# Kernel optimization log

Measured on AMD Instinct MI355X. Metric: run time of the kernel, lower is better.

Reference implementation:

```python
import jax, jax.numpy as jnp
import numpy as np

T, K, N = 4096, 4096, 11008  # tokens, in_features, out_features


def _unpack_int4(packed):
    """packed: int8 [..., K//2] -> signed 4-bit values int8 [..., K].
    Low nibble first, high nibble second; arithmetic shifts sign-extend."""
    lo = jnp.right_shift(jnp.left_shift(packed, 4).astype(jnp.int8), 4)
    hi = jnp.right_shift(packed, 4).astype(jnp.int8)
    out = jnp.stack([lo, hi], axis=-1)  # [..., K//2, 2]
    return out.reshape(*packed.shape[:-1], packed.shape[-1] * 2)


def _pack_int4(vals):
    """vals: int8 in [-8,7], [..., K] -> packed int8 [..., K//2]."""
    v = vals.reshape(*vals.shape[:-1], vals.shape[-1] // 2, 2)
    lo = v[..., 0] & 0xF
    hi = v[..., 1] & 0xF
    return (lo | jnp.left_shift(hi, 4)).astype(jnp.int8)


def setup_inputs() -> dict:
    key = jax.random.key(0)
    k1, k2, k3, k4 = jax.random.split(key, 4)
    # symmetric 4-bit quantized values in [-7, 7], packed two per byte
    x_int = jax.random.randint(k1, (T, K), -7, 8).astype(jnp.int8)
    w_int = jax.random.randint(k2, (N, K), -7, 8).astype(jnp.int8)
    pq_x = _pack_int4(x_int)
    weight = _pack_int4(w_int)
    # per-token / per-output-channel dequant scales (max_abs/7 style magnitudes)
    scales_x = (jax.random.uniform(k3, (T,), jnp.float32) * 0.01 + 1e-4)
    weight_scales = (jax.random.uniform(k4, (N,), jnp.float32) * 0.01 + 1e-4)
    return {"pq_x": pq_x, "scales_x": scales_x, "weight": weight,
            "weight_scales": weight_scales}


def reference(pq_x, scales_x, weight, weight_scales):
    # Unpack int4 operands. Products |a*w| <= 49 and K=4096 => |acc| <= 2e5,
    # exactly representable in fp32, so the fp32 matmul equals int32 GEMM.
    a = _unpack_int4(pq_x).astype(jnp.float32)      # [T, K]
    w = _unpack_int4(weight).astype(jnp.float32)    # [N, K]
    acc = jnp.einsum('tk,nk->tn', a, w)             # integer GEMM in fp32
    # fused per-token x per-output-channel dequant
    out = acc * scales_x[:, None] * weight_scales[None, :]
    out = out.astype(jnp.float16)
    return out[None]  # unsqueeze(0) as in the torch module
```

## Files before the change

### kernel.cpp

```cpp
#include <hip/hip_runtime.h>
#include <hip/hip_fp16.h>
#include <stdint.h>


#define T_DIM 4096
#define K_DIM 4096
#define N_DIM 11008
#define KP    2048
#define BM 128
#define BN 256
#define STAGES 64
#define A_PANELS (T_DIM / BM)
#define B_PANELS (N_DIM / BN)
#define CHUNK_A 8192
#define CHUNK_B 16384
#define WS_A ((size_t)A_PANELS * STAGES * CHUNK_A)
#define WS_B ((size_t)B_PANELS * STAGES * CHUNK_B)
#define NA_BYTES ((size_t)T_DIM * KP)
#define NW_BYTES ((size_t)N_DIM * KP)

typedef __attribute__((ext_vector_type(4)))  int int32x4;
typedef __attribute__((ext_vector_type(16))) int int32x16;
typedef __attribute__((ext_vector_type(4)))  float floatx4;
typedef __attribute__((ext_vector_type(8)))  _Float16 f16x8;
typedef __attribute__((ext_vector_type(2)))  _Float16 f16x2;

__device__ __forceinline__ uint32_t pack4(int4 v) {
  return (uint32_t)(v.x & 0xFF) | ((uint32_t)(v.y & 0xFF) << 8) |
         ((uint32_t)(v.z & 0xFF) << 16) | ((uint32_t)(v.w & 0xFF) << 24);
}
__device__ __forceinline__ uint32_t nib_lo_s8(uint32_t p) {
  uint32_t t = (p & 0x0F0F0F0Fu) ^ 0x88888888u;
  return (t - 0x08080808u) ^ 0x80808080u;
}
__device__ __forceinline__ uint32_t nib_hi_s8(uint32_t p) {
  uint32_t t = ((p >> 4) & 0x0F0F0F0Fu) ^ 0x88888888u;
  return (t - 0x08080808u) ^ 0x80808080u;
}

#define ROWS_PB 32
#define SGRP    16

__global__ __launch_bounds__(256) void unpack_tiles3(
    const int* __restrict__ xa, const int* __restrict__ xw,
    uint8_t* __restrict__ wsa, uint8_t* __restrict__ wsb)
{
  __shared__ __align__(16) uint32_t lds[8192];
  const int sg  = blockIdx.x;
  const int yb  = blockIdx.y;
  const int tid = threadIdx.x;

  const int* srcBase; uint8_t* dstBase; int cellStride, chunkStride;
  if (yb < T_DIM / ROWS_PB) {
    srcBase = xa + (size_t)yb * ROWS_PB * KP + sg * SGRP * 32;
    dstBase = wsa + ((size_t)(yb >> 2) * STAGES + sg * SGRP) * CHUNK_A
                  + (size_t)(yb & 3) * (ROWS_PB * 16);
    cellStride = 2048; chunkStride = CHUNK_A;
  } else {
    const int zb = yb - T_DIM / ROWS_PB;
    srcBase = xw + (size_t)zb * ROWS_PB * KP + sg * SGRP * 32;
    dstBase = wsb + ((size_t)(zb >> 3) * STAGES + sg * SGRP) * CHUNK_B
                  + (size_t)(zb & 7) * (ROWS_PB * 16);
    cellStride = 4096; chunkStride = CHUNK_B;
  }

  const int lq    = tid & 127;
  const int rhalf = tid >> 7;
  const int sl    = lq >> 3;
  const int tg    = lq & 7;
  const int cellL = (tg & 1) * 2;
  const int dsl   = tg >> 1;
#pragma unroll
  for (int it = 0; it < 16; ++it) {
    const int row = it * 2 + rhalf;
    const int4 v = *(const int4*)(srcBase + (size_t)row * KP + lq * 4);
    const uint32_t p = pack4(v);
    const int sp = sl ^ (row & 7);
    uint32_t* b = &lds[(((cellL * 32 + row) << 4) + sp) * 4 + dsl];
    b[0]    = nib_lo_s8(p);
    b[2048] = nib_hi_s8(p);
  }
  __syncthreads();

  const int row2 = tid & 31;
#pragma unroll
  for (int it = 0; it < 8; ++it) {
    const int pr = it * 8 + (tid >> 5);
    const int s2 = pr >> 2, cl = pr & 3;
    const int sp = s2 ^ (row2 & 7);
    const uint4 v = *(const uint4*)&lds[(((cl * 32 + row2) << 4) + sp) * 4];
    *(uint4*)(dstBase + (size_t)s2 * chunkStride + cl * cellStride + row2 * 16) = v;
  }
}

__device__ __forceinline__ void dma16(const uint8_t* g, uint8_t* l) {
  __builtin_amdgcn_global_load_lds(
      (const __attribute__((address_space(1))) uint32_t*)g,
      (__attribute__((address_space(3))) uint32_t*)l, 16, 0, 0);
}

__global__ __launch_bounds__(512, 4) void gemm_i8_tb2(
    const uint8_t* __restrict__ wsa, const uint8_t* __restrict__ wsb,
    const float* __restrict__ sx, const float* __restrict__ sw,
    float* __restrict__ out)
{
  __shared__ __align__(16) uint8_t sAmem[3 * CHUNK_A];
  __shared__ __align__(16) uint8_t sBmem[3 * CHUNK_B];

  const int tid  = threadIdx.x;
  const int lane = tid & 63;
  const int wv   = tid >> 6;
  const int wm   = wv >> 2, wn = wv & 3;
  const int h    = lane >> 5;
  const int ml   = lane & 31;
  const int pp   = blockIdx.x;
  const int qq   = blockIdx.y;

  const uint8_t* chunkA = wsa + (size_t)pp * STAGES * CHUNK_A;
  const uint8_t* chunkB = wsb + (size_t)qq * STAGES * CHUNK_B;
  const int laneOff = lane * 16;
  const int aOffW   = wv * 1024;
  const int bOffW   = wv * 2048;

  const int rowA = (wm * 64 + ml) * 16;
  const int rowB = (wn * 64 + ml) * 16;

  int32x16 acc[2][2];
#pragma unroll
  for (int mi = 0; mi < 2; ++mi)
#pragma unroll
    for (int ni = 0; ni < 2; ++ni)
#pragma unroll
      for (int i = 0; i < 16; ++i) acc[mi][ni][i] = 0;

  auto dma_stage = [&](int s, int buf) {
    const uint8_t* ca = chunkA + (size_t)s * CHUNK_A;
    const uint8_t* cb = chunkB + (size_t)s * CHUNK_B;
    uint8_t* la = sAmem + buf * CHUNK_A;
    uint8_t* lb = sBmem + buf * CHUNK_B;
    dma16(ca + aOffW + laneOff,        la + aOffW);
    dma16(cb + bOffW + laneOff,        lb + bOffW);
    dma16(cb + bOffW + 1024 + laneOff, lb + bOffW + 1024);
  };

  dma_stage(0, 0);
  dma_stage(1, 1);

  int rb = 0;
  int wb = 2;
#pragma unroll 1
  for (int s = 0; s < STAGES; ++s) {
    if (s < STAGES - 1) asm volatile("s_waitcnt vmcnt(3)" ::: "memory");
    else                asm volatile("s_waitcnt vmcnt(0)" ::: "memory");
    __builtin_amdgcn_s_barrier();
    if (s + 2 < STAGES) dma_stage(s + 2, wb);

    const uint8_t* baseA = sAmem + rb * CHUNK_A;
    const uint8_t* baseB = sBmem + rb * CHUNK_B;
#pragma unroll
    for (int s2 = 0; s2 < 2; ++s2) {
      const int c = 2 * s2 + h;
      const uint8_t* pa = baseA + c * 2048 + rowA;
      const uint8_t* pb = baseB + c * 4096 + rowB;
      int32x4 aF[2], bF[2];
#pragma unroll
      for (int mi = 0; mi < 2; ++mi) aF[mi] = *(const int32x4*)(pa + mi * 512);
#pragma unroll
      for (int ni = 0; ni < 2; ++ni) bF[ni] = *(const int32x4*)(pb + ni * 512);
      __builtin_amdgcn_s_setprio(1);
#pragma unroll
      for (int mi = 0; mi < 2; ++mi)
#pragma unroll
        for (int ni = 0; ni < 2; ++ni)
          acc[mi][ni] = __builtin_amdgcn_mfma_i32_32x32x32_i8(
              aF[mi], bF[ni], acc[mi][ni], 0, 0, 0);
      __builtin_amdgcn_s_setprio(0);
    }
    rb = (rb == 2) ? 0 : rb + 1;
    wb = (wb == 2) ? 0 : wb + 1;
  }

#pragma unroll
  for (int mi = 0; mi < 2; ++mi) {
    const int rbase = pp * BM + wm * 64 + mi * 32 + 4 * h;
    float sxv[16];
#pragma unroll
    for (int r = 0; r < 16; ++r) sxv[r] = sx[rbase + (r & 3) + 8 * (r >> 2)];
#pragma unroll
    for (int ni = 0; ni < 2; ++ni) {
      const int gcol = qq * BN + wn * 64 + ni * 32 + ml;
      const float swv = sw[gcol];
#pragma unroll
      for (int r = 0; r < 16; ++r) {
        const int grow = rbase + (r & 3) + 8 * (r >> 2);
        const float v = (float)acc[mi][ni][r] * sxv[r] * swv;
        out[(size_t)grow * N_DIM + gcol] = __half2float(__float2half(v));
      }
    }
  }
}

__global__ __launch_bounds__(256) void repack_int32_to_bytes(
    const int* __restrict__ xa, const int* __restrict__ xw,
    uint32_t* __restrict__ da, uint32_t* __restrict__ dw)
{
  const size_t i = (size_t)blockIdx.x * blockDim.x + threadIdx.x;
  const size_t na4 = NA_BYTES / 4;
  const int4* src; uint32_t* dst; size_t off;
  if (i < na4) { src = (const int4*)xa; dst = da; off = i; }
  else         { src = (const int4*)xw; dst = dw; off = i - na4; }
  const int4 v = src[off];
  dst[off] = pack4(v);
}

__device__ __forceinline__ uint32_t cvt2(uint32_t m) {
  union U { uint32_t u; f16x2 h; } a, b, c;
  a.u = m ^ 0x64086408u; b.u = 0xE408E408u; c.h = a.h + b.h;
  return c.u;
}
__device__ __forceinline__ void unpack_cell(uint32_t* cell, uint32_t p) {
  cell[0] = cvt2( p        & 0x000F000Fu);
  cell[1] = cvt2((p >> 4)  & 0x000F000Fu);
  cell[2] = cvt2((p >> 8)  & 0x000F000Fu);
  cell[3] = cvt2((p >> 12) & 0x000F000Fu);
}

template <bool PACKED>
__global__ __launch_bounds__(256) void linear4bit_f16(
    const uint8_t* __restrict__ pqx, const float* __restrict__ sx,
    const uint8_t* __restrict__ wq,  const float* __restrict__ sw,
    const int* __restrict__ pqx32,   const int* __restrict__ wq32,
    float* __restrict__ out)
{
  __shared__ uint32_t sAf[8][128][4];
  __shared__ uint32_t sBf[8][128][4];
  const int tid = threadIdx.x, lane = tid & 63, wv = tid >> 6;
  const int wm = wv >> 1, wn = wv & 1, qd = lane >> 4, m16 = lane & 15;
  const int bm0 = blockIdx.x * 128, bn0 = blockIdx.y * 128;
  const int srow = tid >> 1, sh = tid & 1;
  const uint8_t* aPtr = pqx + (size_t)(bm0 + srow) * KP + sh * 16;
  const uint8_t* bPtr = wq  + (size_t)(bn0 + srow) * KP + sh * 16;
  const int* aPtr32 = pqx32 + (size_t)(bm0 + srow) * KP + sh * 16;
  const int* bPtr32 = wq32  + (size_t)(bn0 + srow) * KP + sh * 16;
  floatx4 acc[4][4];
#pragma unroll
  for (int mi = 0; mi < 4; ++mi)
#pragma unroll
    for (int ni = 0; ni < 4; ++ni)
#pragma unroll
      for (int r = 0; r < 4; ++r) acc[mi][ni][r] = 0.0f;
  uint4 ar, br;
  auto load_stage = [&](int s) {
    if (PACKED) {
      ar = *(const uint4*)(aPtr + (size_t)s * 32);
      br = *(const uint4*)(bPtr + (size_t)s * 32);
    } else {
      const int4* a4 = (const int4*)(aPtr32 + (size_t)s * 32);
      const int4* b4 = (const int4*)(bPtr32 + (size_t)s * 32);
      ar.x = pack4(a4[0]); ar.y = pack4(a4[1]); ar.z = pack4(a4[2]); ar.w = pack4(a4[3]);
      br.x = pack4(b4[0]); br.y = pack4(b4[1]); br.z = pack4(b4[2]); br.w = pack4(b4[3]);
    }
  };
  auto stage_to_lds = [&]() {
    uint32_t pa[4] = {ar.x, ar.y, ar.z, ar.w};
    uint32_t pb[4] = {br.x, br.y, br.z, br.w};
#pragma unroll
    for (int i = 0; i < 4; ++i) {
      unpack_cell(&sAf[4 * sh + i][srow][0], pa[i]);
      unpack_cell(&sBf[4 * sh + i][srow][0], pb[i]);
    }
  };
  load_stage(0); stage_to_lds();
#pragma unroll 1
  for (int s = 0; s < STAGES; ++s) {
    __syncthreads();
    if (s + 1 < STAGES) load_stage(s + 1);
#pragma unroll
    for (int s2 = 0; s2 < 2; ++s2) {
      f16x8 aF[4], bF[4];
#pragma unroll
      for (int mi = 0; mi < 4; ++mi)
        aF[mi] = *(const f16x8*)&sAf[4 * s2 + qd][wm * 64 + mi * 16 + m16][0];
#pragma unroll
      for (int ni = 0; ni < 4; ++ni)
        bF[ni] = *(const f16x8*)&sBf[4 * s2 + qd][wn * 64 + ni * 16 + m16][0];
#pragma unroll
      for (int mi = 0; mi < 4; ++mi)
#pragma unroll
        for (int ni = 0; ni < 4; ++ni)
          acc[mi][ni] = __builtin_amdgcn_mfma_f32_16x16x32_f16(aF[mi], bF[ni], acc[mi][ni], 0, 0, 0);
    }
    __syncthreads();
    if (s + 1 < STAGES) stage_to_lds();
  }
#pragma unroll
  for (int mi = 0; mi < 4; ++mi) {
    const int grow0 = bm0 + wm * 64 + mi * 16 + qd * 4;
    const float s0 = sx[grow0], s1 = sx[grow0 + 1], s2v = sx[grow0 + 2], s3 = sx[grow0 + 3];
#pragma unroll
    for (int ni = 0; ni < 4; ++ni) {
      const int gcol = bn0 + wn * 64 + ni * 16 + m16;
      const float swv = sw[gcol];
      const floatx4 a = acc[mi][ni];
      out[(size_t)(grow0 + 0) * N_DIM + gcol] = __half2float(__float2half(a[0] * s0 * swv));
      out[(size_t)(grow0 + 1) * N_DIM + gcol] = __half2float(__float2half(a[1] * s1 * swv));
      out[(size_t)(grow0 + 2) * N_DIM + gcol] = __half2float(__float2half(a[2] * s2v * swv));
      out[(size_t)(grow0 + 3) * N_DIM + gcol] = __half2float(__float2half(a[3] * s3 * swv));
    }
  }
}

extern "C" void kernel_launch(void* const* d_in, const int* in_sizes, int n_in,
                              void* d_out, int out_size, void* d_ws, size_t ws_size,
                              hipStream_t stream) {
  const int*   pqx32 = (const int*)d_in[0];
  const float* sxp   = (const float*)d_in[1];
  const int*   wq32  = (const int*)d_in[2];
  const float* swp   = (const float*)d_in[3];
  float* outp = (float*)d_out;

  if (ws_size >= WS_A + WS_B) {
    uint8_t* wsa = (uint8_t*)d_ws;
    uint8_t* wsb = wsa + WS_A;
    unpack_tiles3<<<dim3(STAGES / SGRP, T_DIM / ROWS_PB + N_DIM / ROWS_PB), 256, 0, stream>>>(
        pqx32, wq32, wsa, wsb);
    gemm_i8_tb2<<<dim3(A_PANELS, B_PANELS), 512, 0, stream>>>(wsa, wsb, sxp, swp, outp);
  } else if (ws_size >= NA_BYTES + NW_BYTES) {
    uint8_t* da = (uint8_t*)d_ws;
    uint8_t* dw = da + NA_BYTES;
    const size_t total4 = (NA_BYTES + NW_BYTES) / 4;
    repack_int32_to_bytes<<<(uint32_t)(total4 / 256), 256, 0, stream>>>(
        pqx32, wq32, (uint32_t*)da, (uint32_t*)dw);
    linear4bit_f16<true><<<dim3(T_DIM / 128, N_DIM / 128), 256, 0, stream>>>(
        da, sxp, dw, swp, nullptr, nullptr, outp);
  } else {
    linear4bit_f16<false><<<dim3(T_DIM / 128, N_DIM / 128), 256, 0, stream>>>(
        nullptr, sxp, nullptr, swp, pqx32, wq32, outp);
  }
}
```

Before: 466.8 us.

## Use 4-wave blocks with 2x4 warp tiles and phased DMA/MFMA interleaving

Cuts the GEMM block from 8 to 4 waves, so each wave now computes a 64x128 tile (2x4 MFMA accumulators) rather than 64x64. This gives more register reuse of A fragments. The stage loop is split into four phases, and each phase interleaves a few global-to-LDS DMA issues with one group of MFMAs, separated by extra barriers. The aim is to spread memory traffic across compute, but the extra barriers and the halved thread count per block could lower latency hiding and occupancy.

```diff
diff --git a/kernel.cpp b/kernel.cpp
--- a/kernel.cpp
+++ b/kernel.cpp
@@ -99,7 +99,7 @@
       (__attribute__((address_space(3))) uint32_t*)l, 16, 0, 0);
 }
 
-__global__ __launch_bounds__(512, 4) void gemm_i8_tb2(
+__global__ __launch_bounds__(256, 2) void gemm_i8_ph(
     const uint8_t* __restrict__ wsa, const uint8_t* __restrict__ wsb,
     const float* __restrict__ sx, const float* __restrict__ sw,
     float* __restrict__ out)
@@ -110,7 +110,7 @@
   const int tid  = threadIdx.x;
   const int lane = tid & 63;
   const int wv   = tid >> 6;
-  const int wm   = wv >> 2, wn = wv & 3;
+  const int wm   = wv >> 1, wn = wv & 1;
   const int h    = lane >> 5;
   const int ml   = lane & 31;
   const int pp   = blockIdx.x;
@@ -118,64 +118,102 @@
 
   const uint8_t* chunkA = wsa + (size_t)pp * STAGES * CHUNK_A;
   const uint8_t* chunkB = wsb + (size_t)qq * STAGES * CHUNK_B;
-  const int laneOff = lane * 16;
-  const int aOffW   = wv * 1024;
-  const int bOffW   = wv * 2048;
+  const int segOff = wv * 1024 + lane * 16;
+  const int ldsOff = wv * 1024;
 
   const int rowA = (wm * 64 + ml) * 16;
-  const int rowB = (wn * 64 + ml) * 16;
-
-  int32x16 acc[2][2];
+  const int rowB = (wn * 128 + ml) * 16;
+
+  int32x16 acc[2][4];
 #pragma unroll
   for (int mi = 0; mi < 2; ++mi)
 #pragma unroll
-    for (int ni = 0; ni < 2; ++ni)
+    for (int ni = 0; ni < 4; ++ni)
 #pragma unroll
       for (int i = 0; i < 16; ++i) acc[mi][ni][i] = 0;
 
-  auto dma_stage = [&](int s, int buf) {
-    const uint8_t* ca = chunkA + (size_t)s * CHUNK_A;
-    const uint8_t* cb = chunkB + (size_t)s * CHUNK_B;
-    uint8_t* la = sAmem + buf * CHUNK_A;
-    uint8_t* lb = sBmem + buf * CHUNK_B;
-    dma16(ca + aOffW + laneOff,        la + aOffW);
-    dma16(cb + bOffW + laneOff,        lb + bOffW);
-    dma16(cb + bOffW + 1024 + laneOff, lb + bOffW + 1024);
+  auto dmaA = [&](int s, int buf, int i) {
+    dma16(chunkA + (size_t)s * CHUNK_A + segOff + i * 4096,
+          sAmem + buf * CHUNK_A + ldsOff + i * 4096);
   };
-
-  dma_stage(0, 0);
-  dma_stage(1, 1);
+  auto dmaB = [&](int s, int buf, int i) {
+    dma16(chunkB + (size_t)s * CHUNK_B + segOff + i * 4096,
+          sBmem + buf * CHUNK_B + ldsOff + i * 4096);
+  };
+
+  dmaA(0, 0, 0); dmaA(0, 0, 1);
+  dmaB(0, 0, 0); dmaB(0, 0, 1); dmaB(0, 0, 2); dmaB(0, 0, 3);
+  dmaA(1, 1, 0); dmaA(1, 1, 1);
+  dmaB(1, 1, 0); dmaB(1, 1, 1); dmaB(1, 1, 2); dmaB(1, 1, 3);
 
   int rb = 0;
   int wb = 2;
 #pragma unroll 1
   for (int s = 0; s < STAGES; ++s) {
-    if (s < STAGES - 1) asm volatile("s_waitcnt vmcnt(3)" ::: "memory");
+    if (s < STAGES - 1) asm volatile("s_waitcnt vmcnt(6)" ::: "memory");
     else                asm volatile("s_waitcnt vmcnt(0)" ::: "memory");
     __builtin_amdgcn_s_barrier();
-    if (s + 2 < STAGES) dma_stage(s + 2, wb);
+    const bool pf = (s + 2 < STAGES);
 
     const uint8_t* baseA = sAmem + rb * CHUNK_A;
     const uint8_t* baseB = sBmem + rb * CHUNK_B;
-#pragma unroll
-    for (int s2 = 0; s2 < 2; ++s2) {
-      const int c = 2 * s2 + h;
-      const uint8_t* pa = baseA + c * 2048 + rowA;
-      const uint8_t* pb = baseB + c * 4096 + rowB;
-      int32x4 aF[2], bF[2];
-#pragma unroll
-      for (int mi = 0; mi < 2; ++mi) aF[mi] = *(const int32x4*)(pa + mi * 512);
-#pragma unroll
-      for (int ni = 0; ni < 2; ++ni) bF[ni] = *(const int32x4*)(pb + ni * 512);
-      __builtin_amdgcn_s_setprio(1);
-#pragma unroll
-      for (int mi = 0; mi < 2; ++mi)
-#pragma unroll
-        for (int ni = 0; ni < 2; ++ni)
-          acc[mi][ni] = __builtin_amdgcn_mfma_i32_32x32x32_i8(
-              aF[mi], bF[ni], acc[mi][ni], 0, 0, 0);
-      __builtin_amdgcn_s_setprio(0);
-    }
+    const uint8_t* paL = baseA + h * 2048 + rowA;
+    const uint8_t* pbL = baseB + h * 4096 + rowB;
+    const uint8_t* paH = baseA + (2 + h) * 2048 + rowA;
+    const uint8_t* pbH = baseB + (2 + h) * 4096 + rowB;
+
+    int32x4 a0, a1, b0, b1;
+
+    a0 = *(const int32x4*)(paL);
+    a1 = *(const int32x4*)(paL + 512);
+    b0 = *(const int32x4*)(pbL);
+    b1 = *(const int32x4*)(pbL + 512);
+    if (pf) { dmaA(s + 2, wb, 0); dmaA(s + 2, wb, 1); }
+    __builtin_amdgcn_s_barrier();
+    __builtin_amdgcn_s_setprio(1);
+    acc[0][0] = __builtin_amdgcn_mfma_i32_32x32x32_i8(a0, b0, acc[0][0], 0, 0, 0);
+    acc[1][0] = __builtin_amdgcn_mfma_i32_32x32x32_i8(a1, b0, acc[1][0], 0, 0, 0);
+    acc[0][1] = __builtin_amdgcn_mfma_i32_32x32x32_i8(a0, b1, acc[0][1], 0, 0, 0);
+    acc[1][1] = __builtin_amdgcn_mfma_i32_32x32x32_i8(a1, b1, acc[1][1], 0, 0, 0);
+    __builtin_amdgcn_s_setprio(0);
+    __builtin_amdgcn_s_barrier();
+
+    b0 = *(const int32x4*)(pbL + 1024);
+    b1 = *(const int32x4*)(pbL + 1536);
+    if (pf) { dmaB(s + 2, wb, 0); dmaB(s + 2, wb, 1); }
+    __builtin_amdgcn_s_barrier();
+    __builtin_amdgcn_s_setprio(1);
+    acc[0][2] = __builtin_amdgcn_mfma_i32_32x32x32_i8(a0, b0, acc[0][2], 0, 0, 0);
+    acc[1][2] = __builtin_amdgcn_mfma_i32_32x32x32_i8(a1, b0, acc[1][2], 0, 0, 0);
+    acc[0][3] = __builtin_amdgcn_mfma_i32_32x32x32_i8(a0, b1, acc[0][3], 0, 0, 0);
+    acc[1][3] = __builtin_amdgcn_mfma_i32_32x32x32_i8(a1, b1, acc[1][3], 0, 0, 0);
+    __builtin_amdgcn_s_setprio(0);
+    __builtin_amdgcn_s_barrier();
+
+    a0 = *(const int32x4*)(paH);
+    a1 = *(const int32x4*)(paH + 512);
+    b0 = *(const int32x4*)(pbH);
+    b1 = *(const int32x4*)(pbH + 512);
+    if (pf) { dmaB(s + 2, wb, 2); dmaB(s + 2, wb, 3); }
+    __builtin_amdgcn_s_barrier();
+    __builtin_amdgcn_s_setprio(1);
+    acc[0][0] = __builtin_amdgcn_mfma_i32_32x32x32_i8(a0, b0, acc[0][0], 0, 0, 0);
+    acc[1][0] = __builtin_amdgcn_mfma_i32_32x32x32_i8(a1, b0, acc[1][0], 0, 0, 0);
+    acc[0][1] = __builtin_amdgcn_mfma_i32_32x32x32_i8(a0, b1, acc[0][1], 0, 0, 0);
+    acc[1][1] = __builtin_amdgcn_mfma_i32_32x32x32_i8(a1, b1, acc[1][1], 0, 0, 0);
+    __builtin_amdgcn_s_setprio(0);
+    __builtin_amdgcn_s_barrier();
+
+    b0 = *(const int32x4*)(pbH + 1024);
+    b1 = *(const int32x4*)(pbH + 1536);
+    __builtin_amdgcn_s_barrier();
+    __builtin_amdgcn_s_setprio(1);
+    acc[0][2] = __builtin_amdgcn_mfma_i32_32x32x32_i8(a0, b0, acc[0][2], 0, 0, 0);
+    acc[1][2] = __builtin_amdgcn_mfma_i32_32x32x32_i8(a1, b0, acc[1][2], 0, 0, 0);
+    acc[0][3] = __builtin_amdgcn_mfma_i32_32x32x32_i8(a0, b1, acc[0][3], 0, 0, 0);
+    acc[1][3] = __builtin_amdgcn_mfma_i32_32x32x32_i8(a1, b1, acc[1][3], 0, 0, 0);
+    __builtin_amdgcn_s_setprio(0);
+
     rb = (rb == 2) ? 0 : rb + 1;
     wb = (wb == 2) ? 0 : wb + 1;
   }
@@ -187,8 +225,8 @@
 #pragma unroll
     for (int r = 0; r < 16; ++r) sxv[r] = sx[rbase + (r & 3) + 8 * (r >> 2)];
 #pragma unroll
-    for (int ni = 0; ni < 2; ++ni) {
-      const int gcol = qq * BN + wn * 64 + ni * 32 + ml;
+    for (int ni = 0; ni < 4; ++ni) {
+      const int gcol = qq * BN + wn * 128 + ni * 32 + ml;
       const float swv = sw[gcol];
 #pragma unroll
       for (int r = 0; r < 16; ++r) {
@@ -324,7 +362,7 @@
     uint8_t* wsb = wsa + WS_A;
     unpack_tiles3<<<dim3(STAGES / SGRP, T_DIM / ROWS_PB + N_DIM / ROWS_PB), 256, 0, stream>>>(
         pqx32, wq32, wsa, wsb);
-    gemm_i8_tb2<<<dim3(A_PANELS, B_PANELS), 512, 0, stream>>>(wsa, wsb, sxp, swp, outp);
+    gemm_i8_ph<<<dim3(A_PANELS, B_PANELS), 256, 0, stream>>>(wsa, wsb, sxp, swp, outp);
   } else if (ws_size >= NA_BYTES + NW_BYTES) {
     uint8_t* da = (uint8_t*)d_ws;
     uint8_t* dw = da + NA_BYTES;
```

After: 469.2 us. No clear change (+0.5%).

## Use 256x256 tiles with 4 waves, 4-deep LDS pipeline and XCD-aware block swizzle

Applied to the files above, without the earlier changes.

Replaces the 128x256 tile GEMM (8 waves, 3-stage buffers) with a 256x256 tile handled by 4 waves, each computing a 128x128 sub-tile of 4x4 MFMA accumulators. Stages are quadruple-buffered, with DMA issued three stages ahead and LDS fragment loads double-buffered in registers so reads overlap the MFMA blocks. Block indices are swizzled across 8 groups so that neighbouring tiles share the same chiplet's L2. The unpack kernel is changed to write A in the same 16 KB chunk layout as B. The larger tile raises reuse per byte loaded, at the cost of very high register pressure and one block per CU.

```diff
diff --git a/kernel.cpp b/kernel.cpp
--- a/kernel.cpp
+++ b/kernel.cpp
@@ -7,15 +7,16 @@
 #define K_DIM 4096
 #define N_DIM 11008
 #define KP    2048
-#define BM 128
-#define BN 256
 #define STAGES 64
-#define A_PANELS (T_DIM / BM)
-#define B_PANELS (N_DIM / BN)
-#define CHUNK_A 8192
-#define CHUNK_B 16384
-#define WS_A ((size_t)A_PANELS * STAGES * CHUNK_A)
-#define WS_B ((size_t)B_PANELS * STAGES * CHUNK_B)
+#define BM2 256
+#define BN2 256
+#define CHUNK2 16384
+#define A_PANELS2 (T_DIM / BM2)
+#define B_PANELS2 (N_DIM / BN2)
+#define NWG2 (A_PANELS2 * B_PANELS2)
+#define CPX2 (NWG2 / 8)
+#define WS_A ((size_t)A_PANELS2 * STAGES * CHUNK2)
+#define WS_B ((size_t)B_PANELS2 * STAGES * CHUNK2)
 #define NA_BYTES ((size_t)T_DIM * KP)
 #define NW_BYTES ((size_t)N_DIM * KP)
 
@@ -41,7 +42,7 @@
 #define ROWS_PB 32
 #define SGRP    16
 
-__global__ __launch_bounds__(256) void unpack_tiles3(
+__global__ __launch_bounds__(256) void unpack_tiles4(
     const int* __restrict__ xa, const int* __restrict__ xw,
     uint8_t* __restrict__ wsa, uint8_t* __restrict__ wsb)
 {
@@ -50,18 +51,16 @@
   const int yb  = blockIdx.y;
   const int tid = threadIdx.x;
 
-  const int* srcBase; uint8_t* dstBase; int cellStride, chunkStride;
+  const int* srcBase; uint8_t* dstBase;
   if (yb < T_DIM / ROWS_PB) {
     srcBase = xa + (size_t)yb * ROWS_PB * KP + sg * SGRP * 32;
-    dstBase = wsa + ((size_t)(yb >> 2) * STAGES + sg * SGRP) * CHUNK_A
-                  + (size_t)(yb & 3) * (ROWS_PB * 16);
-    cellStride = 2048; chunkStride = CHUNK_A;
+    dstBase = wsa + ((size_t)(yb >> 3) * STAGES + sg * SGRP) * CHUNK2
+                  + (size_t)(yb & 7) * (ROWS_PB * 16);
   } else {
     const int zb = yb - T_DIM / ROWS_PB;
     srcBase = xw + (size_t)zb * ROWS_PB * KP + sg * SGRP * 32;
-    dstBase = wsb + ((size_t)(zb >> 3) * STAGES + sg * SGRP) * CHUNK_B
+    dstBase = wsb + ((size_t)(zb >> 3) * STAGES + sg * SGRP) * CHUNK2
                   + (size_t)(zb & 7) * (ROWS_PB * 16);
-    cellStride = 4096; chunkStride = CHUNK_B;
   }
 
   const int lq    = tid & 127;
@@ -89,7 +88,7 @@
     const int s2 = pr >> 2, cl = pr & 3;
     const int sp = s2 ^ (row2 & 7);
     const uint4 v = *(const uint4*)&lds[(((cl * 32 + row2) << 4) + sp) * 4];
-    *(uint4*)(dstBase + (size_t)s2 * chunkStride + cl * cellStride + row2 * 16) = v;
+    *(uint4*)(dstBase + (size_t)s2 * CHUNK2 + cl * 4096 + row2 * 16) = v;
   }
 }
 
@@ -99,96 +98,125 @@
       (__attribute__((address_space(3))) uint32_t*)l, 16, 0, 0);
 }
 
-__global__ __launch_bounds__(512, 4) void gemm_i8_tb2(
+__global__ __launch_bounds__(256, 1) void gemm_i8_sq(
     const uint8_t* __restrict__ wsa, const uint8_t* __restrict__ wsb,
     const float* __restrict__ sx, const float* __restrict__ sw,
     float* __restrict__ out)
 {
-  __shared__ __align__(16) uint8_t sAmem[3 * CHUNK_A];
-  __shared__ __align__(16) uint8_t sBmem[3 * CHUNK_B];
+  __shared__ __align__(16) uint8_t sA[4 * CHUNK2];
+  __shared__ __align__(16) uint8_t sB[4 * CHUNK2];
 
   const int tid  = threadIdx.x;
   const int lane = tid & 63;
   const int wv   = tid >> 6;
-  const int wm   = wv >> 2, wn = wv & 3;
+  const int wm   = wv >> 1, wn = wv & 1;
   const int h    = lane >> 5;
   const int ml   = lane & 31;
-  const int pp   = blockIdx.x;
-  const int qq   = blockIdx.y;
-
-  const uint8_t* chunkA = wsa + (size_t)pp * STAGES * CHUNK_A;
-  const uint8_t* chunkB = wsb + (size_t)qq * STAGES * CHUNK_B;
-  const int laneOff = lane * 16;
-  const int aOffW   = wv * 1024;
-  const int bOffW   = wv * 2048;
-
-  const int rowA = (wm * 64 + ml) * 16;
-  const int rowB = (wn * 64 + ml) * 16;
-
-  int32x16 acc[2][2];
-#pragma unroll
-  for (int mi = 0; mi < 2; ++mi)
-#pragma unroll
-    for (int ni = 0; ni < 2; ++ni)
+
+  const int lin = blockIdx.y * A_PANELS2 + blockIdx.x;
+  const int swz = (lin & 7) * CPX2 + (lin >> 3);
+  const int pp  = swz & (A_PANELS2 - 1);
+  const int qq  = swz >> 4;
+
+  const uint8_t* chunkA = wsa + (size_t)pp * STAGES * CHUNK2;
+  const uint8_t* chunkB = wsb + (size_t)qq * STAGES * CHUNK2;
+
+  const uint8_t* gsrc = (wv < 2) ? chunkA : chunkB;
+  uint8_t* lbase      = (wv < 2) ? sA : sB;
+  const int half      = (wv & 1) * 8192;
+
+  auto dma_stage = [&](int s) {
+    const int buf = s & 3;
+    const uint8_t* g = gsrc + (size_t)s * CHUNK2 + half + lane * 16;
+    uint8_t* l = lbase + buf * CHUNK2 + half;
+#pragma unroll
+    for (int i = 0; i < 8; ++i) dma16(g + i * 1024, l + i * 1024);
+  };
+
+  const int rowA = (wm * 128 + ml) * 16;
+  const int rowB = (wn * 128 + ml) * 16;
+
+  int32x16 acc[4][4];
+#pragma unroll
+  for (int mi = 0; mi < 4; ++mi)
+#pragma unroll
+    for (int ni = 0; ni < 4; ++ni)
 #pragma unroll
       for (int i = 0; i < 16; ++i) acc[mi][ni][i] = 0;
 
-  auto dma_stage = [&](int s, int buf) {
-    const uint8_t* ca = chunkA + (size_t)s * CHUNK_A;
-    const uint8_t* cb = chunkB + (size_t)s * CHUNK_B;
-    uint8_t* la = sAmem + buf * CHUNK_A;
-    uint8_t* lb = sBmem + buf * CHUNK_B;
-    dma16(ca + aOffW + laneOff,        la + aOffW);
-    dma16(cb + bOffW + laneOff,        lb + bOffW);
-    dma16(cb + bOffW + 1024 + laneOff, lb + bOffW + 1024);
-  };
-
-  dma_stage(0, 0);
-  dma_stage(1, 1);
-
-  int rb = 0;
-  int wb = 2;
+  dma_stage(0); dma_stage(1); dma_stage(2);
+  asm volatile("s_waitcnt vmcnt(16)" ::: "memory");
+  __builtin_amdgcn_s_barrier();
+
+  int32x4 a0[4], b0[4];
+  {
+    const uint8_t* pa = sA + h * 4096 + rowA;
+    const uint8_t* pb = sB + h * 4096 + rowB;
+#pragma unroll
+    for (int i = 0; i < 4; ++i) a0[i] = *(const int32x4*)(pa + i * 512);
+#pragma unroll
+    for (int i = 0; i < 4; ++i) b0[i] = *(const int32x4*)(pb + i * 512);
+  }
+
 #pragma unroll 1
   for (int s = 0; s < STAGES; ++s) {
-    if (s < STAGES - 1) asm volatile("s_waitcnt vmcnt(3)" ::: "memory");
+    const int rb = s & 3;
+    if (s < STAGES - 2) asm volatile("s_waitcnt vmcnt(8)" ::: "memory");
     else                asm volatile("s_waitcnt vmcnt(0)" ::: "memory");
     __builtin_amdgcn_s_barrier();
-    if (s + 2 < STAGES) dma_stage(s + 2, wb);
-
-    const uint8_t* baseA = sAmem + rb * CHUNK_A;
-    const uint8_t* baseB = sBmem + rb * CHUNK_B;
-#pragma unroll
-    for (int s2 = 0; s2 < 2; ++s2) {
-      const int c = 2 * s2 + h;
-      const uint8_t* pa = baseA + c * 2048 + rowA;
-      const uint8_t* pb = baseB + c * 4096 + rowB;
-      int32x4 aF[2], bF[2];
-#pragma unroll
-      for (int mi = 0; mi < 2; ++mi) aF[mi] = *(const int32x4*)(pa + mi * 512);
-#pragma unroll
-      for (int ni = 0; ni < 2; ++ni) bF[ni] = *(const int32x4*)(pb + ni * 512);
-      __builtin_amdgcn_s_setprio(1);
-#pragma unroll
-      for (int mi = 0; mi < 2; ++mi)
-#pragma unroll
-        for (int ni = 0; ni < 2; ++ni)
-          acc[mi][ni] = __builtin_amdgcn_mfma_i32_32x32x32_i8(
-              aF[mi], bF[ni], acc[mi][ni], 0, 0, 0);
-      __builtin_amdgcn_s_setprio(0);
-    }
-    rb = (rb == 2) ? 0 : rb + 1;
-    wb = (wb == 2) ? 0 : wb + 1;
-  }
-
-#pragma unroll
-  for (int mi = 0; mi < 2; ++mi) {
-    const int rbase = pp * BM + wm * 64 + mi * 32 + 4 * h;
+    if (s + 3 < STAGES) dma_stage(s + 3);
+
+    const uint8_t* baseA = sA + rb * CHUNK2;
+    const uint8_t* baseB = sB + rb * CHUNK2;
+
+    int32x4 a1[4], b1[4];
+    {
+      const uint8_t* pa = baseA + (2 + h) * 4096 + rowA;
+      const uint8_t* pb = baseB + (2 + h) * 4096 + rowB;
+#pragma unroll
+      for (int i = 0; i < 4; ++i) a1[i] = *(const int32x4*)(pa + i * 512);
+#pragma unroll
+      for (int i = 0; i < 4; ++i) b1[i] = *(const int32x4*)(pb + i * 512);
+    }
+
+    __builtin_amdgcn_s_setprio(1);
+#pragma unroll
+    for (int mi = 0; mi < 4; ++mi)
+#pragma unroll
+      for (int ni = 0; ni < 4; ++ni)
+        acc[mi][ni] = __builtin_amdgcn_mfma_i32_32x32x32_i8(
+            a0[mi], b0[ni], acc[mi][ni], 0, 0, 0);
+    __builtin_amdgcn_s_setprio(0);
+
+    if (s + 1 < STAGES) {
+      const int nb = (s + 1) & 3;
+      const uint8_t* pa = sA + nb * CHUNK2 + h * 4096 + rowA;
+      const uint8_t* pb = sB + nb * CHUNK2 + h * 4096 + rowB;
+#pragma unroll
+      for (int i = 0; i < 4; ++i) a0[i] = *(const int32x4*)(pa + i * 512);
+#pragma unroll
+      for (int i = 0; i < 4; ++i) b0[i] = *(const int32x4*)(pb + i * 512);
+    }
+
+    __builtin_amdgcn_s_setprio(1);
+#pragma unroll
+    for (int mi = 0; mi < 4; ++mi)
+#pragma unroll
+      for (int ni = 0; ni < 4; ++ni)
+        acc[mi][ni] = __builtin_amdgcn_mfma_i32_32x32x32_i8(
+            a1[mi], b1[ni], acc[mi][ni], 0, 0, 0);
+    __builtin_amdgcn_s_setprio(0);
+  }
+
+#pragma unroll
+  for (int mi = 0; mi < 4; ++mi) {
+    const int rbase = pp * BM2 + wm * 128 + mi * 32 + 4 * h;
     float sxv[16];
 #pragma unroll
     for (int r = 0; r < 16; ++r) sxv[r] = sx[rbase + (r & 3) + 8 * (r >> 2)];
 #pragma unroll
-    for (int ni = 0; ni < 2; ++ni) {
-      const int gcol = qq * BN + wn * 64 + ni * 32 + ml;
+    for (int ni = 0; ni < 4; ++ni) {
+      const int gcol = qq * BN2 + wn * 128 + ni * 32 + ml;
       const float swv = sw[gcol];
 #pragma unroll
       for (int r = 0; r < 16; ++r) {
@@ -322,9 +350,9 @@
   if (ws_size >= WS_A + WS_B) {
     uint8_t* wsa = (uint8_t*)d_ws;
     uint8_t* wsb = wsa + WS_A;
-    unpack_tiles3<<<dim3(STAGES / SGRP, T_DIM / ROWS_PB + N_DIM / ROWS_PB), 256, 0, stream>>>(
+    unpack_tiles4<<<dim3(STAGES / SGRP, T_DIM / ROWS_PB + N_DIM / ROWS_PB), 256, 0, stream>>>(
         pqx32, wq32, wsa, wsb);
-    gemm_i8_tb2<<<dim3(A_PANELS, B_PANELS), 512, 0, stream>>>(wsa, wsb, sxp, swp, outp);
+    gemm_i8_sq<<<dim3(A_PANELS2, B_PANELS2), 256, 0, stream>>>(wsa, wsb, sxp, swp, outp);
   } else if (ws_size >= NA_BYTES + NW_BYTES) {
     uint8_t* da = (uint8_t*)d_ws;
     uint8_t* dw = da + NA_BYTES;
```

Result: slower. 746.3 us (+59.9%).

## Fuse int4 unpack into GEMM main loop and swizzle workgroup order

Applied to the files above, without the earlier changes.

Removes the separate unpack/tiling pre-pass and its workspace. The GEMM now loads the raw int32-per-byte packed inputs straight from global memory, sign-extends nibbles in registers and writes them to double-buffered LDS. This replaces the 3-stage direct-to-LDS DMA pipeline with a register-staged two-buffer scheme, and lowers launch bounds occupancy from 4 to 2. A workgroup index swizzle groups tiles for L2 reuse. The risk is that the GEMM loads 4x more bytes per element (int32 storage) repeatedly across N/M panels instead of once, and ALU unpack in the hot loop.

```diff
diff --git a/kernel.cpp b/kernel.cpp
--- a/kernel.cpp
+++ b/kernel.cpp
@@ -12,18 +12,11 @@
 #define STAGES 64
 #define A_PANELS (T_DIM / BM)
 #define B_PANELS (N_DIM / BN)
-#define CHUNK_A 8192
-#define CHUNK_B 16384
-#define WS_A ((size_t)A_PANELS * STAGES * CHUNK_A)
-#define WS_B ((size_t)B_PANELS * STAGES * CHUNK_B)
-#define NA_BYTES ((size_t)T_DIM * KP)
-#define NW_BYTES ((size_t)N_DIM * KP)
+#define NWG (A_PANELS * B_PANELS)
+#define CPX (NWG / 8)
 
 typedef __attribute__((ext_vector_type(4)))  int int32x4;
 typedef __attribute__((ext_vector_type(16))) int int32x16;
-typedef __attribute__((ext_vector_type(4)))  float floatx4;
-typedef __attribute__((ext_vector_type(8)))  _Float16 f16x8;
-typedef __attribute__((ext_vector_type(2)))  _Float16 f16x2;
 
 __device__ __forceinline__ uint32_t pack4(int4 v) {
   return (uint32_t)(v.x & 0xFF) | ((uint32_t)(v.y & 0xFF) << 8) |
@@ -37,75 +30,19 @@
   uint32_t t = ((p >> 4) & 0x0F0F0F0Fu) ^ 0x88888888u;
   return (t - 0x08080808u) ^ 0x80808080u;
 }
-
-#define ROWS_PB 32
-#define SGRP    16
-
-__global__ __launch_bounds__(256) void unpack_tiles3(
-    const int* __restrict__ xa, const int* __restrict__ xw,
-    uint8_t* __restrict__ wsa, uint8_t* __restrict__ wsb)
-{
-  __shared__ __align__(16) uint32_t lds[8192];
-  const int sg  = blockIdx.x;
-  const int yb  = blockIdx.y;
-  const int tid = threadIdx.x;
-
-  const int* srcBase; uint8_t* dstBase; int cellStride, chunkStride;
-  if (yb < T_DIM / ROWS_PB) {
-    srcBase = xa + (size_t)yb * ROWS_PB * KP + sg * SGRP * 32;
-    dstBase = wsa + ((size_t)(yb >> 2) * STAGES + sg * SGRP) * CHUNK_A
-                  + (size_t)(yb & 3) * (ROWS_PB * 16);
-    cellStride = 2048; chunkStride = CHUNK_A;
-  } else {
-    const int zb = yb - T_DIM / ROWS_PB;
-    srcBase = xw + (size_t)zb * ROWS_PB * KP + sg * SGRP * 32;
-    dstBase = wsb + ((size_t)(zb >> 3) * STAGES + sg * SGRP) * CHUNK_B
-                  + (size_t)(zb & 7) * (ROWS_PB * 16);
-    cellStride = 4096; chunkStride = CHUNK_B;
-  }
-
-  const int lq    = tid & 127;
-  const int rhalf = tid >> 7;
-  const int sl    = lq >> 3;
-  const int tg    = lq & 7;
-  const int cellL = (tg & 1) * 2;
-  const int dsl   = tg >> 1;
-#pragma unroll
-  for (int it = 0; it < 16; ++it) {
-    const int row = it * 2 + rhalf;
-    const int4 v = *(const int4*)(srcBase + (size_t)row * KP + lq * 4);
-    const uint32_t p = pack4(v);
-    const int sp = sl ^ (row & 7);
-    uint32_t* b = &lds[(((cellL * 32 + row) << 4) + sp) * 4 + dsl];
-    b[0]    = nib_lo_s8(p);
-    b[2048] = nib_hi_s8(p);
-  }
-  __syncthreads();
-
-  const int row2 = tid & 31;
-#pragma unroll
-  for (int it = 0; it < 8; ++it) {
-    const int pr = it * 8 + (tid >> 5);
-    const int s2 = pr >> 2, cl = pr & 3;
-    const int sp = s2 ^ (row2 & 7);
-    const uint4 v = *(const uint4*)&lds[(((cl * 32 + row2) << 4) + sp) * 4];
-    *(uint4*)(dstBase + (size_t)s2 * chunkStride + cl * cellStride + row2 * 16) = v;
-  }
+__device__ __forceinline__ uint2 nib2(int4 v) {
+  const uint32_t p = pack4(v);
+  return make_uint2(nib_lo_s8(p), nib_hi_s8(p));
 }
 
-__device__ __forceinline__ void dma16(const uint8_t* g, uint8_t* l) {
-  __builtin_amdgcn_global_load_lds(
-      (const __attribute__((address_space(1))) uint32_t*)g,
-      (__attribute__((address_space(3))) uint32_t*)l, 16, 0, 0);
-}
 
-__global__ __launch_bounds__(512, 4) void gemm_i8_tb2(
-    const uint8_t* __restrict__ wsa, const uint8_t* __restrict__ wsb,
+__global__ __launch_bounds__(512, 2) void gemm_i8_fused(
+    const int* __restrict__ xa, const int* __restrict__ xw,
     const float* __restrict__ sx, const float* __restrict__ sw,
     float* __restrict__ out)
 {
-  __shared__ __align__(16) uint8_t sAmem[3 * CHUNK_A];
-  __shared__ __align__(16) uint8_t sBmem[3 * CHUNK_B];
+  __shared__ __align__(16) uint8_t sA[2 * 8192];
+  __shared__ __align__(16) uint8_t sB[2 * 16384];
 
   const int tid  = threadIdx.x;
   const int lane = tid & 63;
@@ -113,14 +50,39 @@
   const int wm   = wv >> 2, wn = wv & 3;
   const int h    = lane >> 5;
   const int ml   = lane & 31;
-  const int pp   = blockIdx.x;
-  const int qq   = blockIdx.y;
 
-  const uint8_t* chunkA = wsa + (size_t)pp * STAGES * CHUNK_A;
-  const uint8_t* chunkB = wsb + (size_t)qq * STAGES * CHUNK_B;
-  const int laneOff = lane * 16;
-  const int aOffW   = wv * 1024;
-  const int bOffW   = wv * 2048;
+  const int lin = blockIdx.y * A_PANELS + blockIdx.x;
+  const int swz = (lin & 7) * CPX + (lin >> 3);
+  const int pp  = swz & (A_PANELS - 1);
+  const int qq  = swz >> 5;
+  const int bm0 = pp * BM, bn0 = qq * BN;
+
+  const int jj = tid & 7;
+  const int r0 = tid >> 3;
+  const int* gA = xa + (size_t)(bm0 + r0) * KP + jj * 4;
+  const int* gB = xw + (size_t)(bn0 + r0) * KP + jj * 4;
+
+  int4 rA[2], rB[4];
+  auto issue = [&](int s) {
+    const int o = s * 32;
+    rA[0] = *(const int4*)(gA + o);
+    rA[1] = *(const int4*)(gA + o + 64 * KP);
+#pragma unroll
+    for (int i = 0; i < 4; ++i)
+      rB[i] = *(const int4*)(gB + o + (size_t)i * 64 * KP);
+  };
+
+  uint8_t* const wA0 = sA + (jj >> 1) * 2048 + r0 * 16 + (jj & 1) * 8;
+  uint8_t* const wB0 = sB + (jj >> 1) * 4096 + r0 * 16 + (jj & 1) * 8;
+  auto stash = [&](int buf) {
+    uint8_t* wa = wA0 + buf * 8192;
+    uint8_t* wb = wB0 + buf * 16384;
+    *(uint2*)(wa)        = nib2(rA[0]);
+    *(uint2*)(wa + 1024) = nib2(rA[1]);
+#pragma unroll
+    for (int i = 0; i < 4; ++i)
+      *(uint2*)(wb + i * 1024) = nib2(rB[i]);
+  };
 
   const int rowA = (wm * 64 + ml) * 16;
   const int rowB = (wn * 64 + ml) * 16;
@@ -133,30 +95,17 @@
 #pragma unroll
       for (int i = 0; i < 16; ++i) acc[mi][ni][i] = 0;
 
-  auto dma_stage = [&](int s, int buf) {
-    const uint8_t* ca = chunkA + (size_t)s * CHUNK_A;
-    const uint8_t* cb = chunkB + (size_t)s * CHUNK_B;
-    uint8_t* la = sAmem + buf * CHUNK_A;
-    uint8_t* lb = sBmem + buf * CHUNK_B;
-    dma16(ca + aOffW + laneOff,        la + aOffW);
-    dma16(cb + bOffW + laneOff,        lb + bOffW);
-    dma16(cb + bOffW + 1024 + laneOff, lb + bOffW + 1024);
-  };
+  issue(0);
+  stash(0);
+  __syncthreads();
 
-  dma_stage(0, 0);
-  dma_stage(1, 1);
-
-  int rb = 0;
-  int wb = 2;
 #pragma unroll 1
   for (int s = 0; s < STAGES; ++s) {
-    if (s < STAGES - 1) asm volatile("s_waitcnt vmcnt(3)" ::: "memory");
-    else                asm volatile("s_waitcnt vmcnt(0)" ::: "memory");
-    __builtin_amdgcn_s_barrier();
-    if (s + 2 < STAGES) dma_stage(s + 2, wb);
+    const int rb = s & 1;
+    if (s + 1 < STAGES) issue(s + 1);
 
-    const uint8_t* baseA = sAmem + rb * CHUNK_A;
-    const uint8_t* baseB = sBmem + rb * CHUNK_B;
+    const uint8_t* baseA = sA + rb * 8192;
+    const uint8_t* baseB = sB + rb * 16384;
 #pragma unroll
     for (int s2 = 0; s2 < 2; ++s2) {
       const int c = 2 * s2 + h;
@@ -176,19 +125,22 @@
               aF[mi], bF[ni], acc[mi][ni], 0, 0, 0);
       __builtin_amdgcn_s_setprio(0);
     }
-    rb = (rb == 2) ? 0 : rb + 1;
-    wb = (wb == 2) ? 0 : wb + 1;
+
+    if (s + 1 < STAGES) {
+      stash(rb ^ 1);
+      __syncthreads();
+    }
   }
 
 #pragma unroll
   for (int mi = 0; mi < 2; ++mi) {
-    const int rbase = pp * BM + wm * 64 + mi * 32 + 4 * h;
+    const int rbase = bm0 + wm * 64 + mi * 32 + 4 * h;
     float sxv[16];
 #pragma unroll
     for (int r = 0; r < 16; ++r) sxv[r] = sx[rbase + (r & 3) + 8 * (r >> 2)];
 #pragma unroll
     for (int ni = 0; ni < 2; ++ni) {
-      const int gcol = qq * BN + wn * 64 + ni * 32 + ml;
+      const int gcol = bn0 + wn * 64 + ni * 32 + ml;
       const float swv = sw[gcol];
 #pragma unroll
       for (int r = 0; r < 16; ++r) {
@@ -196,116 +148,6 @@
         const float v = (float)acc[mi][ni][r] * sxv[r] * swv;
         out[(size_t)grow * N_DIM + gcol] = __half2float(__float2half(v));
       }
-    }
-  }
-}
-
-__global__ __launch_bounds__(256) void repack_int32_to_bytes(
-    const int* __restrict__ xa, const int* __restrict__ xw,
-    uint32_t* __restrict__ da, uint32_t* __restrict__ dw)
-{
-  const size_t i = (size_t)blockIdx.x * blockDim.x + threadIdx.x;
-  const size_t na4 = NA_BYTES / 4;
-  const int4* src; uint32_t* dst; size_t off;
-  if (i < na4) { src = (const int4*)xa; dst = da; off = i; }
-  else         { src = (const int4*)xw; dst = dw; off = i - na4; }
-  const int4 v = src[off];
-  dst[off] = pack4(v);
-}
-
-__device__ __forceinline__ uint32_t cvt2(uint32_t m) {
-  union U { uint32_t u; f16x2 h; } a, b, c;
-  a.u = m ^ 0x64086408u; b.u = 0xE408E408u; c.h = a.h + b.h;
-  return c.u;
-}
-__device__ __forceinline__ void unpack_cell(uint32_t* cell, uint32_t p) {
-  cell[0] = cvt2( p        & 0x000F000Fu);
-  cell[1] = cvt2((p >> 4)  & 0x000F000Fu);
-  cell[2] = cvt2((p >> 8)  & 0x000F000Fu);
-  cell[3] = cvt2((p >> 12) & 0x000F000Fu);
-}
-
-template <bool PACKED>
-__global__ __launch_bounds__(256) void linear4bit_f16(
-    const uint8_t* __restrict__ pqx, const float* __restrict__ sx,
-    const uint8_t* __restrict__ wq,  const float* __restrict__ sw,
-    const int* __restrict__ pqx32,   const int* __restrict__ wq32,
-    float* __restrict__ out)
-{
-  __shared__ uint32_t sAf[8][128][4];
-  __shared__ uint32_t sBf[8][128][4];
-  const int tid = threadIdx.x, lane = tid & 63, wv = tid >> 6;
-  const int wm = wv >> 1, wn = wv & 1, qd = lane >> 4, m16 = lane & 15;
-  const int bm0 = blockIdx.x * 128, bn0 = blockIdx.y * 128;
-  const int srow = tid >> 1, sh = tid & 1;
-  const uint8_t* aPtr = pqx + (size_t)(bm0 + srow) * KP + sh * 16;
-  const uint8_t* bPtr = wq  + (size_t)(bn0 + srow) * KP + sh * 16;
-  const int* aPtr32 = pqx32 + (size_t)(bm0 + srow) * KP + sh * 16;
-  const int* bPtr32 = wq32  + (size_t)(bn0 + srow) * KP + sh * 16;
-  floatx4 acc[4][4];
-#pragma unroll
-  for (int mi = 0; mi < 4; ++mi)
-#pragma unroll
-    for (int ni = 0; ni < 4; ++ni)
-#pragma unroll
-      for (int r = 0; r < 4; ++r) acc[mi][ni][r] = 0.0f;
-  uint4 ar, br;
-  auto load_stage = [&](int s) {
-    if (PACKED) {
-      ar = *(const uint4*)(aPtr + (size_t)s * 32);
-      br = *(const uint4*)(bPtr + (size_t)s * 32);
-    } else {
-      const int4* a4 = (const int4*)(aPtr32 + (size_t)s * 32);
-      const int4* b4 = (const int4*)(bPtr32 + (size_t)s * 32);
-      ar.x = pack4(a4[0]); ar.y = pack4(a4[1]); ar.z = pack4(a4[2]); ar.w = pack4(a4[3]);
-      br.x = pack4(b4[0]); br.y = pack4(b4[1]); br.z = pack4(b4[2]); br.w = pack4(b4[3]);
-    }
-  };
-  auto stage_to_lds = [&]() {
-    uint32_t pa[4] = {ar.x, ar.y, ar.z, ar.w};
-    uint32_t pb[4] = {br.x, br.y, br.z, br.w};
-#pragma unroll
-    for (int i = 0; i < 4; ++i) {
-      unpack_cell(&sAf[4 * sh + i][srow][0], pa[i]);
-      unpack_cell(&sBf[4 * sh + i][srow][0], pb[i]);
-    }
-  };
-  load_stage(0); stage_to_lds();
-#pragma unroll 1
-  for (int s = 0; s < STAGES; ++s) {
-    __syncthreads();
-    if (s + 1 < STAGES) load_stage(s + 1);
-#pragma unroll
-    for (int s2 = 0; s2 < 2; ++s2) {
-      f16x8 aF[4], bF[4];
-#pragma unroll
-      for (int mi = 0; mi < 4; ++mi)
-        aF[mi] = *(const f16x8*)&sAf[4 * s2 + qd][wm * 64 + mi * 16 + m16][0];
-#pragma unroll
-      for (int ni = 0; ni < 4; ++ni)
-        bF[ni] = *(const f16x8*)&sBf[4 * s2 + qd][wn * 64 + ni * 16 + m16][0];
-#pragma unroll
-      for (int mi = 0; mi < 4; ++mi)
-#pragma unroll
-        for (int ni = 0; ni < 4; ++ni)
-          acc[mi][ni] = __builtin_amdgcn_mfma_f32_16x16x32_f16(aF[mi], bF[ni], acc[mi][ni], 0, 0, 0);
-    }
-    __syncthreads();
-    if (s + 1 < STAGES) stage_to_lds();
-  }
-#pragma unroll
-  for (int mi = 0; mi < 4; ++mi) {
-    const int grow0 = bm0 + wm * 64 + mi * 16 + qd * 4;
-    const float s0 = sx[grow0], s1 = sx[grow0 + 1], s2v = sx[grow0 + 2], s3 = sx[grow0 + 3];
-#pragma unroll
-    for (int ni = 0; ni < 4; ++ni) {
-      const int gcol = bn0 + wn * 64 + ni * 16 + m16;
-      const float swv = sw[gcol];
-      const floatx4 a = acc[mi][ni];
-      out[(size_t)(grow0 + 0) * N_DIM + gcol] = __half2float(__float2half(a[0] * s0 * swv));
-      out[(size_t)(grow0 + 1) * N_DIM + gcol] = __half2float(__float2half(a[1] * s1 * swv));
-      out[(size_t)(grow0 + 2) * N_DIM + gcol] = __half2float(__float2half(a[2] * s2v * swv));
-      out[(size_t)(grow0 + 3) * N_DIM + gcol] = __half2float(__float2half(a[3] * s3 * swv));
     }
   }
 }
@@ -319,22 +161,7 @@
   const float* swp   = (const float*)d_in[3];
   float* outp = (float*)d_out;
 
-  if (ws_size >= WS_A + WS_B) {
-    uint8_t* wsa = (uint8_t*)d_ws;
-    uint8_t* wsb = wsa + WS_A;
-    unpack_tiles3<<<dim3(STAGES / SGRP, T_DIM / ROWS_PB + N_DIM / ROWS_PB), 256, 0, stream>>>(
-        pqx32, wq32, wsa, wsb);
-    gemm_i8_tb2<<<dim3(A_PANELS, B_PANELS), 512, 0, stream>>>(wsa, wsb, sxp, swp, outp);
-  } else if (ws_size >= NA_BYTES + NW_BYTES) {
-    uint8_t* da = (uint8_t*)d_ws;
-    uint8_t* dw = da + NA_BYTES;
-    const size_t total4 = (NA_BYTES + NW_BYTES) / 4;
-    repack_int32_to_bytes<<<(uint32_t)(total4 / 256), 256, 0, stream>>>(
-        pqx32, wq32, (uint32_t*)da, (uint32_t*)dw);
-    linear4bit_f16<true><<<dim3(T_DIM / 128, N_DIM / 128), 256, 0, stream>>>(
-        da, sxp, dw, swp, nullptr, nullptr, outp);
-  } else {
-    linear4bit_f16<false><<<dim3(T_DIM / 128, N_DIM / 128), 256, 0, stream>>>(
-        nullptr, sxp, nullptr, swp, pqx32, wq32, outp);
-  }
+  (void)d_ws; (void)ws_size;
+  gemm_i8_fused<<<dim3(A_PANELS, B_PANELS), 512, 0, stream>>>(
+      pqx32, wq32, sxp, swp, outp);
 }
```

Result: slower. 631.0 us (+35.2%).
